# Kernel optimization log

Hardware: AMD Instinct MI355X
Metric: run time of the kernel (lower is better)

The kernel has to match this reference:

```python
import jax, jax.numpy as jnp
import numpy as np

B, NPG, E_PER = 64, 1024, 16384   # graphs per batch, nodes per graph, edges per graph
IN, HID, OUT = 64, 128, 32
N = B * NPG


def setup_inputs() -> dict:
    key = jax.random.key(0)
    ks = jax.random.split(key, 10)
    off = (jnp.arange(B, dtype=jnp.int32) * NPG)[:, None]
    # block-diagonal edges (DGL batched graph: edges stay within each subgraph)
    src = (jax.random.randint(ks[0], (B, E_PER), 0, NPG, jnp.int32) + off).reshape(-1)
    dst = (jax.random.randint(ks[1], (B, E_PER), 0, NPG, jnp.int32) + off).reshape(-1)
    features = jax.random.normal(ks[2], (N, IN), jnp.float32)
    noise = jax.random.normal(ks[3], (N, OUT), jnp.float32)
    glorot = lambda k, i, o: jax.random.normal(k, (i, o), jnp.float32) * np.sqrt(2.0 / (i + o))
    return {
        'features': features, 'src': src, 'dst': dst, 'noise': noise,
        'W1': glorot(ks[4], IN, HID),  'b1': jnp.zeros((HID,), jnp.float32),
        'W2': glorot(ks[5], HID, OUT), 'b2': jnp.zeros((OUT,), jnp.float32),
        'W3': glorot(ks[6], HID, OUT), 'b3': jnp.zeros((OUT,), jnp.float32),
    }


def _gconv(h, src, dst, W, b, n):
    # DGL GraphConv, norm='both': D_out^{-1/2} scale, sum-aggregate src->dst, D_in^{-1/2} scale, linear
    ones = jnp.ones(src.shape[0], h.dtype)
    deg_out = jnp.maximum(jax.ops.segment_sum(ones, src, num_segments=n), 1.0)
    deg_in = jnp.maximum(jax.ops.segment_sum(ones, dst, num_segments=n), 1.0)
    h = h * jax.lax.rsqrt(deg_out)[:, None]
    m = jax.ops.segment_sum(h[src], dst, num_segments=n)   # irregular gather + scatter-add
    m = m * jax.lax.rsqrt(deg_in)[:, None]
    return m @ W + b


def reference(features, src, dst, noise, W1, b1, W2, b2, W3, b3):
    n = features.shape[0]
    h = jax.nn.relu(_gconv(features, src, dst, W1, b1, n))
    mean = _gconv(h, src, dst, W2, b2, n)
    log_std = _gconv(h, src, dst, W3, b3, n)
    z = mean + noise * jnp.exp(log_std)                    # reparameterization
    zb = z.reshape(B, NPG, OUT)
    adj_rec = jax.nn.sigmoid(jnp.einsum('bnd,bmd->bnm', zb, zb))  # per-graph sigmoid(z z^T)
    return adj_rec, mean.reshape(B, NPG, OUT), log_std.reshape(B, NPG, OUT)
```

## Files before the change

### kernel.cpp

```cpp
#include <hip/hip_runtime.h>

constexpr int NB   = 64;
constexpr int NPG  = 1024;
constexpr int EPG  = 16384;
constexpr int NTOT = NB * NPG;
constexpr int ETOT = NB * EPG;
constexpr int FIN  = 64;
constexpr int FHID = 128;
constexpr int FOUT = 32;

__global__ __launch_bounds__(1024) void k_deg(
    const int* __restrict__ src, const int* __restrict__ dst,
    int* __restrict__ dego, int* __restrict__ degi) {
  __shared__ int so[NPG], si[NPG];
  const int g = blockIdx.x, q = blockIdx.y;
  for (int i = threadIdx.x; i < NPG; i += 1024) { so[i] = 0; si[i] = 0; }
  __syncthreads();
  const int eb = g * EPG + q * (EPG / 4);
  const int gb = g * NPG;
  for (int e = threadIdx.x; e < EPG / 4; e += 1024) {
    atomicAdd(&so[src[eb + e] - gb], 1);
    atomicAdd(&si[dst[eb + e] - gb], 1);
  }
  __syncthreads();
  for (int i = threadIdx.x; i < NPG; i += 1024) {
    if (so[i]) atomicAdd(&dego[gb + i], so[i]);
    if (si[i]) atomicAdd(&degi[gb + i], si[i]);
  }
}

__global__ void k_scales(const int* __restrict__ dego, const int* __restrict__ degi,
                         float* __restrict__ rso, float* __restrict__ rsi) {
  int i = blockIdx.x * blockDim.x + threadIdx.x;
  if (i < NTOT) {
    int a = dego[i] > 1 ? dego[i] : 1;
    int b = degi[i] > 1 ? degi[i] : 1;
    rso[i] = rsqrtf((float)a);
    rsi[i] = rsqrtf((float)b);
  }
}

__global__ __launch_bounds__(1024) void k_scan(
    const int* __restrict__ degi, int* __restrict__ ptr, int* __restrict__ cursor) {
  __shared__ int s[NPG];
  const int g = blockIdx.x, t = threadIdx.x;
  const int d = degi[g * NPG + t];
  s[t] = d;
  __syncthreads();
  for (int off = 1; off < NPG; off <<= 1) {
    int v = (t >= off) ? s[t - off] : 0;
    __syncthreads();
    s[t] += v;
    __syncthreads();
  }
  const int p = g * EPG + (s[t] - d);
  ptr[g * NPG + t] = p;
  cursor[g * NPG + t] = p;
  if (g == 0 && t == 0) ptr[NTOT] = ETOT;
}

__global__ void k_fill(const int* __restrict__ src, const int* __restrict__ dst,
                       int* __restrict__ cursor, int* __restrict__ csr) {
  int e = blockIdx.x * blockDim.x + threadIdx.x;
  if (e < ETOT) {
    int d = dst[e];
    int pos = atomicAdd(&cursor[d], 1);
    csr[pos] = src[e];
  }
}

__global__ void k_prefold(const float* __restrict__ features,
                          const int* __restrict__ dego, float* __restrict__ x1) {
  int t = blockIdx.x * blockDim.x + threadIdx.x;
  int node = t >> 4, q = t & 15;
  int dg = dego[node];
  float sc = rsqrtf((float)(dg > 1 ? dg : 1));
  float4 v = *(const float4*)&features[(size_t)node * FIN + q * 4];
  v.x *= sc; v.y *= sc; v.z *= sc; v.w *= sc;
  *(float4*)&x1[(size_t)node * FIN + q * 4] = v;
}

__global__ __launch_bounds__(256) void k_agg_csr(
    const int* __restrict__ ptr, const int* __restrict__ csr,
    const float* __restrict__ x, const float* __restrict__ rsi,
    float* __restrict__ out) {
  const int nblk = gridDim.x;
  const int bid  = blockIdx.x;
  const int swz  = (bid & 7) * (nblk >> 3) + (bid >> 3);
  const int node = swz * 4 + (threadIdx.x >> 6);
  const int lane = threadIdx.x & 63;

  const int start = ptr[node];
  const int end   = ptr[node + 1];
  const int deg   = end - start;

  float acc = 0.0f;
  const float* xb = x + lane;
  if (deg > 0) {
    const int jm = deg < 64 ? deg : 64;
    const int idxv = csr[start + (lane < jm ? lane : 0)];
    for (int j = 0; j < jm; j += 8) {
      int   sj[8];
      float vj[8];
#pragma unroll
      for (int u = 0; u < 8; ++u) {
        int l = j + u;
        sj[u] = __builtin_amdgcn_readlane(idxv, l < jm ? l : 0);
      }
#pragma unroll
      for (int u = 0; u < 8; ++u) vj[u] = xb[(size_t)sj[u] * FIN];
#pragma unroll
      for (int u = 0; u < 8; ++u) acc += (j + u < jm) ? vj[u] : 0.0f;
    }
    for (int e = start + 64; e < end; ++e) acc += xb[(size_t)csr[e] * FIN];
  }
  out[(size_t)node * FIN + lane] = acc * rsi[node];
}

__global__ __launch_bounds__(256) void k_agg2(
    const int* __restrict__ ptr, const int* __restrict__ csr,
    const float* __restrict__ x, const float* __restrict__ rsi,
    const float* __restrict__ b2, const float* __restrict__ b3,
    float* __restrict__ mean_, float* __restrict__ logstd_) {
  const int nblk = gridDim.x;
  const int bid  = blockIdx.x;
  const int swz  = (bid & 7) * (nblk >> 3) + (bid >> 3);
  const int node = swz * 4 + (threadIdx.x >> 6);
  const int lane = threadIdx.x & 63;

  const int start = ptr[node];
  const int end   = ptr[node + 1];
  const int deg   = end - start;

  float acc = 0.0f;
  const float* xb = x + lane;
  if (deg > 0) {
    const int jm = deg < 64 ? deg : 64;
    const int idxv = csr[start + (lane < jm ? lane : 0)];
    for (int j = 0; j < jm; j += 8) {
      int   sj[8];
      float vj[8];
#pragma unroll
      for (int u = 0; u < 8; ++u) {
        int l = j + u;
        sj[u] = __builtin_amdgcn_readlane(idxv, l < jm ? l : 0);
      }
#pragma unroll
      for (int u = 0; u < 8; ++u) vj[u] = xb[(size_t)sj[u] * FIN];
#pragma unroll
      for (int u = 0; u < 8; ++u) acc += (j + u < jm) ? vj[u] : 0.0f;
    }
    for (int e = start + 64; e < end; ++e) acc += xb[(size_t)csr[e] * FIN];
  }
  const float bias = (lane < FOUT) ? b2[lane] : b3[lane - FOUT];
  const float v = acc * rsi[node] + bias;
  if (lane < FOUT) mean_[(size_t)node * FOUT + lane] = v;
  else             logstd_[(size_t)node * FOUT + (lane - FOUT)] = v;
}

__global__ __launch_bounds__(256) void k_gemm1(
    const float* __restrict__ m1, const float* __restrict__ rso,
    const float* __restrict__ W1, const float* __restrict__ b1,
    float* __restrict__ h) {
  __shared__ float sA[FIN][64];
  __shared__ float sW[FIN * FHID];
  __shared__ float sB[FHID];
  const int t = threadIdx.x;
  const int node0 = blockIdx.x * 64;
  for (int f = t; f < FIN * FHID / 4; f += 256)
    ((float4*)sW)[f] = ((const float4*)W1)[f];
  if (t < FHID) sB[t] = b1[t];
  for (int f = t; f < 64 * (FIN / 4); f += 256) {
    int node = f & 63, kq = f >> 6;
    size_t idx = (size_t)(node0 + node) * FIN + kq * 4;
    float4 va = *(const float4*)&m1[idx];
    sA[kq * 4 + 0][node] = va.x;
    sA[kq * 4 + 1][node] = va.y;
    sA[kq * 4 + 2][node] = va.z;
    sA[kq * 4 + 3][node] = va.w;
  }
  __syncthreads();
  const int tx = t & 15, ty = t >> 4;
  float acc[4][8];
#pragma unroll
  for (int r = 0; r < 4; ++r)
#pragma unroll
    for (int c = 0; c < 8; ++c) acc[r][c] = 0.0f;
#pragma unroll 4
  for (int k = 0; k < FIN; ++k) {
    float4 a  = *(float4*)&sA[k][ty * 4];
    float4 w0 = *(float4*)&sW[k * FHID + tx * 8];
    float4 w1 = *(float4*)&sW[k * FHID + tx * 8 + 4];
    float av[4] = {a.x, a.y, a.z, a.w};
    float wv[8] = {w0.x, w0.y, w0.z, w0.w, w1.x, w1.y, w1.z, w1.w};
#pragma unroll
    for (int r = 0; r < 4; ++r)
#pragma unroll
      for (int c = 0; c < 8; ++c) acc[r][c] = fmaf(av[r], wv[c], acc[r][c]);
  }
#pragma unroll
  for (int r = 0; r < 4; ++r) {
    int node = node0 + ty * 4 + r;
    float sc = rso[node];
    float4 o0, o1;
    o0.x = fmaxf(acc[r][0] + sB[tx * 8 + 0], 0.f) * sc;
    o0.y = fmaxf(acc[r][1] + sB[tx * 8 + 1], 0.f) * sc;
    o0.z = fmaxf(acc[r][2] + sB[tx * 8 + 2], 0.f) * sc;
    o0.w = fmaxf(acc[r][3] + sB[tx * 8 + 3], 0.f) * sc;
    o1.x = fmaxf(acc[r][4] + sB[tx * 8 + 4], 0.f) * sc;
    o1.y = fmaxf(acc[r][5] + sB[tx * 8 + 5], 0.f) * sc;
    o1.z = fmaxf(acc[r][6] + sB[tx * 8 + 6], 0.f) * sc;
    o1.w = fmaxf(acc[r][7] + sB[tx * 8 + 7], 0.f) * sc;
    *(float4*)&h[(size_t)node * FHID + tx * 8]     = o0;
    *(float4*)&h[(size_t)node * FHID + tx * 8 + 4] = o1;
  }
}

__global__ __launch_bounds__(256) void k_gemm2(
    const float* __restrict__ h, const float* __restrict__ W2,
    const float* __restrict__ W3, float* __restrict__ p) {
  __shared__ float sA[FHID][64];
  __shared__ float sW[FHID * 64];
  const int t = threadIdx.x;
  const int node0 = blockIdx.x * 64;
  for (int f = t; f < FHID * FOUT / 4; f += 256) {
    int k = f >> 3, jq = f & 7;
    *(float4*)&sW[k * 64 + jq * 4]      = *(const float4*)&W2[k * FOUT + jq * 4];
  }
  for (int f = t; f < FHID * FOUT / 4; f += 256) {
    int k = f >> 3, jq = f & 7;
    *(float4*)&sW[k * 64 + 32 + jq * 4] = *(const float4*)&W3[k * FOUT + jq * 4];
  }
  for (int f = t; f < 64 * (FHID / 4); f += 256) {
    int node = f & 63, kq = f >> 6;
    float4 v = *(const float4*)&h[(size_t)(node0 + node) * FHID + kq * 4];
    sA[kq * 4 + 0][node] = v.x;
    sA[kq * 4 + 1][node] = v.y;
    sA[kq * 4 + 2][node] = v.z;
    sA[kq * 4 + 3][node] = v.w;
  }
  __syncthreads();
  const int tx = t & 15, ty = t >> 4;
  float acc[4][4];
#pragma unroll
  for (int r = 0; r < 4; ++r)
#pragma unroll
    for (int c = 0; c < 4; ++c) acc[r][c] = 0.0f;
#pragma unroll 4
  for (int k = 0; k < FHID; ++k) {
    float4 a = *(float4*)&sA[k][ty * 4];
    float4 w = *(float4*)&sW[k * 64 + tx * 4];
    float av[4] = {a.x, a.y, a.z, a.w};
    float wv[4] = {w.x, w.y, w.z, w.w};
#pragma unroll
    for (int r = 0; r < 4; ++r)
#pragma unroll
      for (int c = 0; c < 4; ++c) acc[r][c] = fmaf(av[r], wv[c], acc[r][c]);
  }
#pragma unroll
  for (int r = 0; r < 4; ++r) {
    float4 o = {acc[r][0], acc[r][1], acc[r][2], acc[r][3]};
    *(float4*)&p[(size_t)(node0 + ty * 4 + r) * 64 + tx * 4] = o;
  }
}

__global__ __launch_bounds__(256) void k_adj(
    const float* __restrict__ mean_, const float* __restrict__ logstd_,
    const float* __restrict__ noise, float* __restrict__ adj) {
  __shared__ float sR[FOUT][128];
  __shared__ float sC[FOUT][128];
  const int g  = blockIdx.z;
  const int c0 = blockIdx.x * 128;
  const int r0 = blockIdx.y * 128;
  const int t  = threadIdx.x;
  const size_t gb = (size_t)g * NPG;
  for (int f = t; f < 2048; f += 256) {
    int half = f >> 10;
    int ff   = f & 1023;
    int node = ff & 127, kq = ff >> 7;
    int base = half ? c0 : r0;
    size_t idx = (gb + base + node) * FOUT + kq * 4;
    float4 m  = *(const float4*)&mean_[idx];
    float4 l  = *(const float4*)&logstd_[idx];
    float4 nz = *(const float4*)&noise[idx];
    float* s = half ? &sC[0][0] : &sR[0][0];
    s[(kq * 4 + 0) * 128 + node] = m.x + nz.x * __expf(l.x);
    s[(kq * 4 + 1) * 128 + node] = m.y + nz.y * __expf(l.y);
    s[(kq * 4 + 2) * 128 + node] = m.z + nz.z * __expf(l.z);
    s[(kq * 4 + 3) * 128 + node] = m.w + nz.w * __expf(l.w);
  }
  __syncthreads();
  const int tx = t & 15, ty = t >> 4;
  float acc[8][8];
#pragma unroll
  for (int r = 0; r < 8; ++r)
#pragma unroll
    for (int c = 0; c < 8; ++c) acc[r][c] = 0.0f;
#pragma unroll 2
  for (int k = 0; k < FOUT; ++k) {
    float4 a0 = *(const float4*)&sR[k][ty * 8];
    float4 a1 = *(const float4*)&sR[k][ty * 8 + 4];
    float4 q0 = *(const float4*)&sC[k][tx * 4];
    float4 q1 = *(const float4*)&sC[k][tx * 4 + 64];
    float av[8] = {a0.x, a0.y, a0.z, a0.w, a1.x, a1.y, a1.z, a1.w};
    float cv[8] = {q0.x, q0.y, q0.z, q0.w, q1.x, q1.y, q1.z, q1.w};
#pragma unroll
    for (int r = 0; r < 8; ++r)
#pragma unroll
      for (int c = 0; c < 8; ++c) acc[r][c] = fmaf(av[r], cv[c], acc[r][c]);
  }
#pragma unroll
  for (int r = 0; r < 8; ++r) {
    size_t row = gb + r0 + ty * 8 + r;
    float4 s0, s1;
    s0.x = __builtin_amdgcn_rcpf(1.0f + __expf(-acc[r][0]));
    s0.y = __builtin_amdgcn_rcpf(1.0f + __expf(-acc[r][1]));
    s0.z = __builtin_amdgcn_rcpf(1.0f + __expf(-acc[r][2]));
    s0.w = __builtin_amdgcn_rcpf(1.0f + __expf(-acc[r][3]));
    s1.x = __builtin_amdgcn_rcpf(1.0f + __expf(-acc[r][4]));
    s1.y = __builtin_amdgcn_rcpf(1.0f + __expf(-acc[r][5]));
    s1.z = __builtin_amdgcn_rcpf(1.0f + __expf(-acc[r][6]));
    s1.w = __builtin_amdgcn_rcpf(1.0f + __expf(-acc[r][7]));
    *(float4*)&adj[row * NPG + c0 + tx * 4]      = s0;
    *(float4*)&adj[row * NPG + c0 + 64 + tx * 4] = s1;
  }
}

extern "C" void kernel_launch(void* const* d_in, const int* in_sizes, int n_in,
                              void* d_out, int out_size, void* d_ws, size_t ws_size,
                              hipStream_t stream) {
  const float* features = (const float*)d_in[0];
  const int*   src      = (const int*)d_in[1];
  const int*   dst      = (const int*)d_in[2];
  const float* noise    = (const float*)d_in[3];
  const float* W1       = (const float*)d_in[4];
  const float* b1       = (const float*)d_in[5];
  const float* W2       = (const float*)d_in[6];
  const float* b2       = (const float*)d_in[7];
  const float* W3       = (const float*)d_in[8];
  const float* b3       = (const float*)d_in[9];

  float* adj     = (float*)d_out;
  float* mean_   = adj + (size_t)NB * NPG * NPG;
  float* logstd_ = mean_ + (size_t)NTOT * FOUT;

  float* x1   = adj;
  float* m1   = x1 + (size_t)NTOT * FIN;
  float* h    = m1 + (size_t)NTOT * FIN;
  float* p    = h + (size_t)NTOT * FHID;
  int*   dego = (int*)(p + (size_t)NTOT * FIN);
  int*   degi = dego + NTOT;
  float* rso  = (float*)(degi + NTOT);
  float* rsi  = rso + NTOT;
  int*   ptr  = (int*)(rsi + NTOT);
  int*   cur  = ptr + (NTOT + 1);
  int*   csr  = cur + NTOT;

  hipMemsetAsync(dego, 0, (size_t)2 * NTOT * sizeof(int), stream);
  k_deg<<<dim3(NB, 4), 1024, 0, stream>>>(src, dst, dego, degi);
  k_scales<<<NTOT / 256, 256, 0, stream>>>(dego, degi, rso, rsi);
  k_scan<<<NB, 1024, 0, stream>>>(degi, ptr, cur);
  k_fill<<<ETOT / 256, 256, 0, stream>>>(src, dst, cur, csr);
  k_prefold<<<NTOT * 16 / 256, 256, 0, stream>>>(features, dego, x1);
  k_agg_csr<<<NTOT / 4, 256, 0, stream>>>(ptr, csr, x1, rsi, m1);
  k_gemm1<<<NTOT / 64, 256, 0, stream>>>(m1, rso, W1, b1, h);
  k_gemm2<<<NTOT / 64, 256, 0, stream>>>(h, W2, W3, p);
  k_agg2<<<NTOT / 4, 256, 0, stream>>>(ptr, csr, p, rsi, b2, b3, mean_, logstd_);
  k_adj<<<dim3(NPG / 128, NPG / 128, NB), 256, 0, stream>>>(mean_, logstd_, noise, adj);
}
```

Before: 528.7 us.

## Fuse graph preprocessing into one kernel and fuse both GEMMs via LDS

```diff
diff --git a/kernel.cpp b/kernel.cpp
--- a/kernel.cpp
+++ b/kernel.cpp
@@ -9,72 +9,49 @@
 constexpr int FHID = 128;
 constexpr int FOUT = 32;
 
-__global__ __launch_bounds__(1024) void k_deg(
+__global__ __launch_bounds__(1024) void k_graph(
     const int* __restrict__ src, const int* __restrict__ dst,
-    int* __restrict__ dego, int* __restrict__ degi) {
-  __shared__ int so[NPG], si[NPG];
-  const int g = blockIdx.x, q = blockIdx.y;
-  for (int i = threadIdx.x; i < NPG; i += 1024) { so[i] = 0; si[i] = 0; }
-  __syncthreads();
-  const int eb = g * EPG + q * (EPG / 4);
-  const int gb = g * NPG;
-  for (int e = threadIdx.x; e < EPG / 4; e += 1024) {
+    float* __restrict__ rso, float* __restrict__ rsi,
+    int* __restrict__ ptr, int* __restrict__ csr) {
+  __shared__ int so[NPG], si[NPG], sc[NPG], cur[NPG];
+  const int g = blockIdx.x, t = threadIdx.x;
+  const int eb = g * EPG, gb = g * NPG;
+  so[t] = 0; si[t] = 0;
+  __syncthreads();
+  for (int e = t; e < EPG; e += 1024) {
     atomicAdd(&so[src[eb + e] - gb], 1);
     atomicAdd(&si[dst[eb + e] - gb], 1);
   }
   __syncthreads();
-  for (int i = threadIdx.x; i < NPG; i += 1024) {
-    if (so[i]) atomicAdd(&dego[gb + i], so[i]);
-    if (si[i]) atomicAdd(&degi[gb + i], si[i]);
-  }
-}
-
-__global__ void k_scales(const int* __restrict__ dego, const int* __restrict__ degi,
-                         float* __restrict__ rso, float* __restrict__ rsi) {
-  int i = blockIdx.x * blockDim.x + threadIdx.x;
-  if (i < NTOT) {
-    int a = dego[i] > 1 ? dego[i] : 1;
-    int b = degi[i] > 1 ? degi[i] : 1;
-    rso[i] = rsqrtf((float)a);
-    rsi[i] = rsqrtf((float)b);
-  }
-}
-
-__global__ __launch_bounds__(1024) void k_scan(
-    const int* __restrict__ degi, int* __restrict__ ptr, int* __restrict__ cursor) {
-  __shared__ int s[NPG];
-  const int g = blockIdx.x, t = threadIdx.x;
-  const int d = degi[g * NPG + t];
-  s[t] = d;
+  const int dgo = so[t];
+  const int dgi = si[t];
+  rso[gb + t] = rsqrtf((float)(dgo > 1 ? dgo : 1));
+  rsi[gb + t] = rsqrtf((float)(dgi > 1 ? dgi : 1));
+  sc[t] = dgi;
   __syncthreads();
   for (int off = 1; off < NPG; off <<= 1) {
-    int v = (t >= off) ? s[t - off] : 0;
+    int v = (t >= off) ? sc[t - off] : 0;
     __syncthreads();
-    s[t] += v;
+    sc[t] += v;
     __syncthreads();
   }
-  const int p = g * EPG + (s[t] - d);
-  ptr[g * NPG + t] = p;
-  cursor[g * NPG + t] = p;
+  const int loc = sc[t] - dgi;
+  ptr[gb + t] = eb + loc;
+  cur[t] = loc;
   if (g == 0 && t == 0) ptr[NTOT] = ETOT;
-}
-
-__global__ void k_fill(const int* __restrict__ src, const int* __restrict__ dst,
-                       int* __restrict__ cursor, int* __restrict__ csr) {
-  int e = blockIdx.x * blockDim.x + threadIdx.x;
-  if (e < ETOT) {
-    int d = dst[e];
-    int pos = atomicAdd(&cursor[d], 1);
-    csr[pos] = src[e];
+  __syncthreads();
+  for (int e = t; e < EPG; e += 1024) {
+    int d = dst[eb + e] - gb;
+    int pos = atomicAdd(&cur[d], 1);
+    csr[eb + pos] = src[eb + e];
   }
 }
 
 __global__ void k_prefold(const float* __restrict__ features,
-                          const int* __restrict__ dego, float* __restrict__ x1) {
+                          const float* __restrict__ rso, float* __restrict__ x1) {
   int t = blockIdx.x * blockDim.x + threadIdx.x;
   int node = t >> 4, q = t & 15;
-  int dg = dego[node];
-  float sc = rsqrtf((float)(dg > 1 ? dg : 1));
+  float sc = rso[node];
   float4 v = *(const float4*)&features[(size_t)node * FIN + q * 4];
   v.x *= sc; v.y *= sc; v.z *= sc; v.w *= sc;
   *(float4*)&x1[(size_t)node * FIN + q * 4] = v;
@@ -158,17 +135,20 @@
   else             logstd_[(size_t)node * FOUT + (lane - FOUT)] = v;
 }
 
-__global__ __launch_bounds__(256) void k_gemm1(
+__global__ __launch_bounds__(256) void k_gemm12(
     const float* __restrict__ m1, const float* __restrict__ rso,
     const float* __restrict__ W1, const float* __restrict__ b1,
-    float* __restrict__ h) {
+    const float* __restrict__ W2, const float* __restrict__ W3,
+    float* __restrict__ p) {
   __shared__ float sA[FIN][64];
-  __shared__ float sW[FIN * FHID];
+  __shared__ float sW1[FIN * FHID];
   __shared__ float sB[FHID];
+  __shared__ float sH[FHID][64];
+  __shared__ float sW23[FHID * 64];
   const int t = threadIdx.x;
   const int node0 = blockIdx.x * 64;
   for (int f = t; f < FIN * FHID / 4; f += 256)
-    ((float4*)sW)[f] = ((const float4*)W1)[f];
+    ((float4*)sW1)[f] = ((const float4*)W1)[f];
   if (t < FHID) sB[t] = b1[t];
   for (int f = t; f < 64 * (FIN / 4); f += 256) {
     int node = f & 63, kq = f >> 6;
@@ -179,88 +159,72 @@
     sA[kq * 4 + 2][node] = va.z;
     sA[kq * 4 + 3][node] = va.w;
   }
-  __syncthreads();
-  const int tx = t & 15, ty = t >> 4;
-  float acc[4][8];
-#pragma unroll
-  for (int r = 0; r < 4; ++r)
-#pragma unroll
-    for (int c = 0; c < 8; ++c) acc[r][c] = 0.0f;
-#pragma unroll 4
-  for (int k = 0; k < FIN; ++k) {
-    float4 a  = *(float4*)&sA[k][ty * 4];
-    float4 w0 = *(float4*)&sW[k * FHID + tx * 8];
-    float4 w1 = *(float4*)&sW[k * FHID + tx * 8 + 4];
-    float av[4] = {a.x, a.y, a.z, a.w};
-    float wv[8] = {w0.x, w0.y, w0.z, w0.w, w1.x, w1.y, w1.z, w1.w};
-#pragma unroll
-    for (int r = 0; r < 4; ++r)
-#pragma unroll
-      for (int c = 0; c < 8; ++c) acc[r][c] = fmaf(av[r], wv[c], acc[r][c]);
-  }
-#pragma unroll
-  for (int r = 0; r < 4; ++r) {
-    int node = node0 + ty * 4 + r;
-    float sc = rso[node];
-    float4 o0, o1;
-    o0.x = fmaxf(acc[r][0] + sB[tx * 8 + 0], 0.f) * sc;
-    o0.y = fmaxf(acc[r][1] + sB[tx * 8 + 1], 0.f) * sc;
-    o0.z = fmaxf(acc[r][2] + sB[tx * 8 + 2], 0.f) * sc;
-    o0.w = fmaxf(acc[r][3] + sB[tx * 8 + 3], 0.f) * sc;
-    o1.x = fmaxf(acc[r][4] + sB[tx * 8 + 4], 0.f) * sc;
-    o1.y = fmaxf(acc[r][5] + sB[tx * 8 + 5], 0.f) * sc;
-    o1.z = fmaxf(acc[r][6] + sB[tx * 8 + 6], 0.f) * sc;
-    o1.w = fmaxf(acc[r][7] + sB[tx * 8 + 7], 0.f) * sc;
-    *(float4*)&h[(size_t)node * FHID + tx * 8]     = o0;
-    *(float4*)&h[(size_t)node * FHID + tx * 8 + 4] = o1;
-  }
-}
-
-__global__ __launch_bounds__(256) void k_gemm2(
-    const float* __restrict__ h, const float* __restrict__ W2,
-    const float* __restrict__ W3, float* __restrict__ p) {
-  __shared__ float sA[FHID][64];
-  __shared__ float sW[FHID * 64];
-  const int t = threadIdx.x;
-  const int node0 = blockIdx.x * 64;
   for (int f = t; f < FHID * FOUT / 4; f += 256) {
     int k = f >> 3, jq = f & 7;
-    *(float4*)&sW[k * 64 + jq * 4]      = *(const float4*)&W2[k * FOUT + jq * 4];
+    *(float4*)&sW23[k * 64 + jq * 4]      = *(const float4*)&W2[k * FOUT + jq * 4];
   }
   for (int f = t; f < FHID * FOUT / 4; f += 256) {
     int k = f >> 3, jq = f & 7;
-    *(float4*)&sW[k * 64 + 32 + jq * 4] = *(const float4*)&W3[k * FOUT + jq * 4];
-  }
-  for (int f = t; f < 64 * (FHID / 4); f += 256) {
-    int node = f & 63, kq = f >> 6;
-    float4 v = *(const float4*)&h[(size_t)(node0 + node) * FHID + kq * 4];
-    sA[kq * 4 + 0][node] = v.x;
-    sA[kq * 4 + 1][node] = v.y;
-    sA[kq * 4 + 2][node] = v.z;
-    sA[kq * 4 + 3][node] = v.w;
+    *(float4*)&sW23[k * 64 + 32 + jq * 4] = *(const float4*)&W3[k * FOUT + jq * 4];
   }
   __syncthreads();
   const int tx = t & 15, ty = t >> 4;
-  float acc[4][4];
-#pragma unroll
-  for (int r = 0; r < 4; ++r)
-#pragma unroll
-    for (int c = 0; c < 4; ++c) acc[r][c] = 0.0f;
+  {
+    float acc[4][8];
+#pragma unroll
+    for (int r = 0; r < 4; ++r)
+#pragma unroll
+      for (int c = 0; c < 8; ++c) acc[r][c] = 0.0f;
 #pragma unroll 4
-  for (int k = 0; k < FHID; ++k) {
-    float4 a = *(float4*)&sA[k][ty * 4];
-    float4 w = *(float4*)&sW[k * 64 + tx * 4];
-    float av[4] = {a.x, a.y, a.z, a.w};
-    float wv[4] = {w.x, w.y, w.z, w.w};
+    for (int k = 0; k < FIN; ++k) {
+      float4 a  = *(float4*)&sA[k][ty * 4];
+      float4 w0 = *(float4*)&sW1[k * FHID + tx * 8];
+      float4 w1 = *(float4*)&sW1[k * FHID + tx * 8 + 4];
+      float av[4] = {a.x, a.y, a.z, a.w};
+      float wv[8] = {w0.x, w0.y, w0.z, w0.w, w1.x, w1.y, w1.z, w1.w};
+#pragma unroll
+      for (int r = 0; r < 4; ++r)
+#pragma unroll
+        for (int c = 0; c < 8; ++c) acc[r][c] = fmaf(av[r], wv[c], acc[r][c]);
+    }
+    float s0 = rso[node0 + ty * 4 + 0];
+    float s1 = rso[node0 + ty * 4 + 1];
+    float s2 = rso[node0 + ty * 4 + 2];
+    float s3 = rso[node0 + ty * 4 + 3];
+#pragma unroll
+    for (int c = 0; c < 8; ++c) {
+      float b = sB[tx * 8 + c];
+      float4 v;
+      v.x = fmaxf(acc[0][c] + b, 0.f) * s0;
+      v.y = fmaxf(acc[1][c] + b, 0.f) * s1;
+      v.z = fmaxf(acc[2][c] + b, 0.f) * s2;
+      v.w = fmaxf(acc[3][c] + b, 0.f) * s3;
+      *(float4*)&sH[tx * 8 + c][ty * 4] = v;
+    }
+  }
+  __syncthreads();
+  {
+    float acc[4][4];
 #pragma unroll
     for (int r = 0; r < 4; ++r)
 #pragma unroll
-      for (int c = 0; c < 4; ++c) acc[r][c] = fmaf(av[r], wv[c], acc[r][c]);
-  }
-#pragma unroll
-  for (int r = 0; r < 4; ++r) {
-    float4 o = {acc[r][0], acc[r][1], acc[r][2], acc[r][3]};
-    *(float4*)&p[(size_t)(node0 + ty * 4 + r) * 64 + tx * 4] = o;
+      for (int c = 0; c < 4; ++c) acc[r][c] = 0.0f;
+#pragma unroll 4
+    for (int k = 0; k < FHID; ++k) {
+      float4 a = *(float4*)&sH[k][ty * 4];
+      float4 w = *(float4*)&sW23[k * 64 + tx * 4];
+      float av[4] = {a.x, a.y, a.z, a.w};
+      float wv[4] = {w.x, w.y, w.z, w.w};
+#pragma unroll
+      for (int r = 0; r < 4; ++r)
+#pragma unroll
+        for (int c = 0; c < 4; ++c) acc[r][c] = fmaf(av[r], wv[c], acc[r][c]);
+    }
+#pragma unroll
+    for (int r = 0; r < 4; ++r) {
+      float4 o = {acc[r][0], acc[r][1], acc[r][2], acc[r][3]};
+      *(float4*)&p[(size_t)(node0 + ty * 4 + r) * 64 + tx * 4] = o;
+    }
   }
 }
 
@@ -346,25 +310,16 @@
 
   float* x1   = adj;
   float* m1   = x1 + (size_t)NTOT * FIN;
-  float* h    = m1 + (size_t)NTOT * FIN;
-  float* p    = h + (size_t)NTOT * FHID;
-  int*   dego = (int*)(p + (size_t)NTOT * FIN);
-  int*   degi = dego + NTOT;
-  float* rso  = (float*)(degi + NTOT);
+  float* p    = m1 + (size_t)NTOT * FIN;
+  float* rso  = p + (size_t)NTOT * FIN;
   float* rsi  = rso + NTOT;
   int*   ptr  = (int*)(rsi + NTOT);
-  int*   cur  = ptr + (NTOT + 1);
-  int*   csr  = cur + NTOT;
-
-  hipMemsetAsync(dego, 0, (size_t)2 * NTOT * sizeof(int), stream);
-  k_deg<<<dim3(NB, 4), 1024, 0, stream>>>(src, dst, dego, degi);
-  k_scales<<<NTOT / 256, 256, 0, stream>>>(dego, degi, rso, rsi);
-  k_scan<<<NB, 1024, 0, stream>>>(degi, ptr, cur);
-  k_fill<<<ETOT / 256, 256, 0, stream>>>(src, dst, cur, csr);
-  k_prefold<<<NTOT * 16 / 256, 256, 0, stream>>>(features, dego, x1);
+  int*   csr  = ptr + (NTOT + 1);
+
+  k_graph<<<NB, 1024, 0, stream>>>(src, dst, rso, rsi, ptr, csr);
+  k_prefold<<<NTOT * 16 / 256, 256, 0, stream>>>(features, rso, x1);
   k_agg_csr<<<NTOT / 4, 256, 0, stream>>>(ptr, csr, x1, rsi, m1);
-  k_gemm1<<<NTOT / 64, 256, 0, stream>>>(m1, rso, W1, b1, h);
-  k_gemm2<<<NTOT / 64, 256, 0, stream>>>(h, W2, W3, p);
+  k_gemm12<<<NTOT / 64, 256, 0, stream>>>(m1, rso, W1, b1, W2, W3, p);
   k_agg2<<<NTOT / 4, 256, 0, stream>>>(ptr, csr, p, rsi, b2, b3, mean_, logstd_);
   k_adj<<<dim3(NPG / 128, NPG / 128, NB), 256, 0, stream>>>(mean_, logstd_, noise, adj);
 }
```

Measured after the change: 516.6 us. -2.3%, faster.
